# Optimization experiments

Hardware: AMD Instinct MI355X
Metric: run time of the kernel (lower is better)

The kernel has to match this reference:

```python
import jax, jax.numpy as jnp
import numpy as np

B, T, EMB, N_HEADS = 2, 2048, 128, 8
K_HALF = 4                      # k: gaussians at offsets -k..k
G_ADD = 2                       # gadditional global samples per gaussian
M = 2 * K_HALF + 1              # 9 gaussians per query
P = M * (2 + G_ADD)             # 36 sparse points per query (2 nearest ints + G_ADD)
SIGMA_BOOST = 2.0
EPS = 1e-7


def setup_inputs() -> dict:
    key = jax.random.key(0)
    ks = jax.random.split(key, 8)
    s = 1.0 / np.sqrt(EMB)
    return {
        "x": jax.random.normal(ks[0], (B, T, EMB), jnp.float32),
        "stride_params": jax.random.uniform(ks[1], (2,), jnp.float32, 0.5, 3.0),  # (dilation, raw sigma)
        "mvalues": jnp.ones((M,), jnp.float32),
        "Wq": jax.random.normal(ks[2], (EMB, EMB * N_HEADS), jnp.float32) * s,
        "Wk": jax.random.normal(ks[3], (EMB, EMB * N_HEADS), jnp.float32) * s,
        "Wv": jax.random.normal(ks[4], (EMB, EMB * N_HEADS), jnp.float32) * s,
        "Wu": jax.random.normal(ks[5], (EMB * N_HEADS, EMB), jnp.float32) * s,
        "bu": jnp.zeros((EMB,), jnp.float32),
    }


def _forward(x, stride_params, mvalues, Wq, Wk, Wv, Wu, bu):
    b, t, emb = x.shape
    dilation, sigma_raw = stride_params[0], stride_params[1]

    # --- hyper(): per-query gaussian means/sigmas (transform_means 'clamp', transform_sigmas softplus) ---
    offsets = jnp.arange(-K_HALF, K_HALF + 1, dtype=x.dtype) * dilation            # (M,)
    pos = jnp.arange(t, dtype=x.dtype)
    means = jnp.clip(pos[None, :, None] + offsets[None, None, :], 0.0, t - 1.0)    # (1,t,M)
    means = jnp.broadcast_to(means, (b, t, M))
    sigma = jax.nn.softplus(sigma_raw + SIGMA_BOOST) + EPS
    sigmas = jnp.broadcast_to(sigma, means.shape)                                  # (b,t,M)

    # --- sparse.ngenerate: 2 nearest ints + G_ADD uniform global samples per gaussian ---
    fl = jnp.floor(means)
    near = jnp.stack([fl, fl + 1.0], axis=-1)                                      # (b,t,M,2)
    glob = jax.random.randint(jax.random.key(42), (b, t, M, G_ADD), 0, t).astype(x.dtype)
    pts = jnp.clip(jnp.concatenate([near, glob], axis=-1), 0.0, t - 1.0)           # (b,t,M,2+G)
    idx = pts.reshape(b, t, P).astype(jnp.int32)                                   # (b,t,P)
    pts_fl = idx.astype(x.dtype)

    # --- sparse.densities: density of each point under each of the M gaussians ---
    diff = (pts_fl[..., :, None] - means[..., None, :]) / sigmas[..., None, :]     # (b,t,P,M)
    dens = jnp.exp(-0.5 * diff * diff)

    # --- util.nduplicates: zero all densities of duplicate points (keep first occurrence) ---
    eq = idx[..., :, None] == idx[..., None, :]                                    # (b,t,i,p)
    earlier = jnp.triu(jnp.ones((P, P), dtype=bool), k=1)                          # i < p
    dup = jnp.any(eq & earlier, axis=-2)                                           # (b,t,P)
    dens = jnp.where(dup[..., None], 0.0, dens)
    dens = dens / dens.sum(axis=2, keepdims=True)                                  # normalize over points per gaussian
    weights = jnp.einsum('btpm,m->btp', dens, mvalues)                             # (b,t,P)

    # --- projections; note per-head dim == emb in this module ---
    def proj(W):
        return jnp.transpose((x @ W).reshape(b, t, N_HEADS, emb), (0, 2, 1, 3))    # (b,h,t,e)

    scale = emb ** 0.25
    Q = proj(Wq) / scale
    K = proj(Wk) / scale
    V = proj(Wv)

    def per_batch(Qb, Kb, Vb, idxb, wb):
        Kg = Kb[:, idxb]                                # (h,t,P,e) irregular gather
        dot = jnp.einsum('hte,htpe->htp', Qb, Kg)       # util.calc_vals: sparse gather dot-products
        attn = jax.nn.softmax(wb[None, :, :] * dot, axis=-1)  # sparse.logsoftmax(...).exp(): per output-row
        Vg = Vb[:, idxb]                                # (h,t,P,e)
        return jnp.einsum('htp,htpe->hte', attn, Vg)    # sparse.batchmm scatter-reduce over rows

    out = jax.vmap(per_batch)(Q, K, V, idx, weights)    # (b,h,t,e)
    out = jnp.transpose(out, (0, 2, 1, 3)).reshape(b, t, N_HEADS * emb)
    return out @ Wu + bu


def reference(x, stride_params, mvalues, Wq, Wk, Wv, Wu, bu):
    return _forward(x, stride_params, mvalues, Wq, Wk, Wv, Wu, bu)
```

## Files before the change

### kernel.cpp

```cpp
#include <hip/hip_runtime.h>
#include <math.h>

#define B_    2
#define T_    2048
#define EMB_  128
#define NH_   8
#define M_    9
#define P_    36
#define GADD_ 2

typedef _Float16 f16;
typedef __attribute__((ext_vector_type(2))) _Float16 f16x2;
typedef __attribute__((ext_vector_type(4))) _Float16 f16x4;
typedef __attribute__((ext_vector_type(8))) _Float16 f16x8;
typedef __attribute__((ext_vector_type(4))) float f32x4;

__device__ __forceinline__ unsigned rotl32(unsigned x, int r){ return (x<<r)|(x>>(32-r)); }

struct U2 { unsigned x, y; };

__device__ __forceinline__ U2 tf2x32(U2 key, U2 ctr){
  unsigned ks[3] = { key.x, key.y, key.x ^ key.y ^ 0x1BD11BDAu };
  unsigned x0 = ctr.x + ks[0], x1 = ctr.y + ks[1];
  const int rotA[4] = {13,15,26,6}, rotB[4] = {17,29,16,24};
  #pragma unroll
  for (int r = 0; r < 5; ++r){
    const int* rr = (r & 1) ? rotB : rotA;
    #pragma unroll
    for (int i = 0; i < 4; ++i){ x0 += x1; x1 = rotl32(x1, rr[i]); x1 ^= x0; }
    x0 += ks[(r+1)%3];
    x1 += ks[(r+2)%3] + (unsigned)(r+1);
  }
  return { x0, x1 };
}

__device__ unsigned glob_rand(unsigned f){
  U2 k2 = tf2x32({0u, 42u}, {0u, 1u});
  U2 o  = tf2x32(k2, {0u, f});
  return (o.x ^ o.y) & (unsigned)(T_-1);
}

__device__ __forceinline__ f16x2 as_f16x2(unsigned u){ return __builtin_bit_cast(f16x2, u); }
__device__ __forceinline__ unsigned as_u32(f16x2 v){ return __builtin_bit_cast(unsigned, v); }

__device__ __forceinline__ void tconv_body(const float* __restrict__ A,
    f16* __restrict__ o, int R, int C, int r0, int c0, float scale,
    float (*tile)[33]){
  const int tx = threadIdx.x & 31, ty = threadIdx.x >> 5;
  #pragma unroll
  for (int i = 0; i < 32; i += 8)
    tile[ty+i][tx] = A[(size_t)(r0+ty+i)*C + c0+tx];
  __syncthreads();
  #pragma unroll
  for (int i = 0; i < 32; i += 8)
    o[(size_t)(c0+ty+i)*R + (r0+tx)] = (f16)(tile[tx][ty+i] * scale);
}

__global__ __launch_bounds__(256) void prep_kernel(
    const float* __restrict__ x, f16* __restrict__ xh,
    const float* __restrict__ Wq, const float* __restrict__ Wk, const float* __restrict__ Wv,
    f16* __restrict__ WT,
    const float* __restrict__ Wu, f16* __restrict__ WuT,
    const float* __restrict__ sp, const float* __restrict__ mvals,
    int* __restrict__ idx_out, float* __restrict__ w_out){
  __shared__ float tile[32][33];
  __shared__ int   s_idx[4][P_];
  __shared__ float s_dens[4][P_][M_];
  __shared__ float s_col[4][M_];
  const int bid = blockIdx.x;
  const float sc = 0.29730177875068026f;

  if (bid < 512){
    const int i = (bid*256 + threadIdx.x)*4;
    float4 v = *(const float4*)(x + i);
    f16x4 p = { (f16)v.x, (f16)v.y, (f16)v.z, (f16)v.w };
    *(f16x4*)(xh + i) = p;
    return;
  }
  if (bid < 896){
    const int zz = bid - 512;
    const int z = zz >> 7, rem = zz & 127;
    const int by = rem >> 5, bx = rem & 31;
    const float* A = (z==0) ? Wq : (z==1) ? Wk : Wv;
    tconv_body(A, WT + (size_t)z*1024*128, 128, 1024, by*32, bx*32, (z<2)?sc:1.0f, tile);
    return;
  }
  if (bid < 1024){
    const int idx2 = bid - 896;
    const int by = idx2 >> 2, bx = idx2 & 3;
    tconv_body(Wu, WuT, 1024, 128, by*32, bx*32, 1.0f, tile);
    return;
  }

  const int g  = threadIdx.x >> 6;
  const int p  = threadIdx.x & 63;
  const int bt = (bid - 1024)*4 + g;
  const int t  = bt & (T_-1);

  const float dil  = sp[0];
  const float xs   = sp[1] + 2.0f;
  const float sigma = xs + log1pf(expf(-xs)) + 1e-7f;

  if (p < P_){
    const int m = p >> 2, j = p & 3;
    const float mean = fminf(fmaxf((float)t + (float)(m-4)*dil, 0.f), (float)(T_-1));
    int id;
    if      (j == 0) id = (int)floorf(mean);
    else if (j == 1) id = min((int)floorf(mean) + 1, T_-1);
    else {
      const unsigned f = ((unsigned)bt * M_ + (unsigned)m) * GADD_ + (unsigned)(j-2);
      id = (int)glob_rand(f);
    }
    s_idx[g][p] = id;
  }
  __syncthreads();
  if (p < P_){
    const int myid = s_idx[g][p];
    bool dup = false;
    for (int q = 0; q < p; ++q) dup |= (s_idx[g][q] == myid);
    const float pf = (float)myid;
    #pragma unroll
    for (int m = 0; m < M_; ++m){
      const float mean = fminf(fmaxf((float)t + (float)(m-4)*dil, 0.f), (float)(T_-1));
      const float d = (pf - mean) / sigma;
      s_dens[g][p][m] = dup ? 0.f : expf(-0.5f * d * d);
    }
  }
  __syncthreads();
  if (p < M_){
    float s = 0.f;
    for (int q = 0; q < P_; ++q) s += s_dens[g][q][p];
    s_col[g][p] = s;
  }
  __syncthreads();
  if (p < P_){
    float w = 0.f;
    #pragma unroll
    for (int m = 0; m < M_; ++m) w += s_dens[g][p][m] / s_col[g][m] * mvals[m];
    idx_out[bt*P_ + p] = s_idx[g][p];
    w_out[bt*P_ + p]   = w;
  }
}

__global__ __launch_bounds__(256) void qkv_mfma_kernel(const f16* __restrict__ xh,
    const f16* __restrict__ WT,
    f16* __restrict__ Qh, f16* __restrict__ Kh, f16* __restrict__ Vh){
  const int w  = threadIdx.x >> 6, l = threadIdx.x & 63;
  const int m0 = blockIdx.y*64 + w*16;
  const int n0 = blockIdx.x*64;
  const int lr = l & 15, lk = l >> 4;

  f16x8 a[4];
  #pragma unroll
  for (int kc = 0; kc < 4; ++kc)
    a[kc] = *(const f16x8*)(xh + (size_t)(m0+lr)*128 + kc*32 + lk*8);

  #pragma unroll
  for (int z = 0; z < 3; ++z){
    const f16* __restrict__ WTz = WT + (size_t)z * 1024 * 128;
    f16* __restrict__ Outh = (z==0) ? Qh : (z==1) ? Kh : Vh;
    f32x4 acc[4] = {};
    #pragma unroll
    for (int nf = 0; nf < 4; ++nf){
      #pragma unroll
      for (int kc = 0; kc < 4; ++kc){
        f16x8 b = *(const f16x8*)(WTz + (size_t)(n0+nf*16+lr)*128 + kc*32 + lk*8);
        acc[nf] = __builtin_amdgcn_mfma_f32_16x16x32_f16(a[kc], b, acc[nf], 0, 0, 0);
      }
    }
    #pragma unroll
    for (int nf = 0; nf < 4; ++nf){
      const int col = n0 + nf*16 + lr;
      #pragma unroll
      for (int r = 0; r < 4; ++r)
        Outh[(size_t)(m0 + lk*4 + r)*1024 + col] = (f16)acc[nf][r];
    }
  }
}

#define RSTR 37
#define NHB  4
__global__ __launch_bounds__(256) void attn_kernel(const f16* __restrict__ Qh,
    const f16* __restrict__ K, const f16* __restrict__ V,
    const int* __restrict__ idx, const float* __restrict__ wts,
    f16* __restrict__ outh){
  const int bid = blockIdx.x;
  const int bt  = ((bid & 7) << 9) | (bid >> 3);
  const int b   = bt >> 11;
  const int hw   = threadIdx.x >> 6, lane = threadIdx.x & 63;
  const int h    = blockIdx.y*NHB + hw;
  const int pg = lane >> 4, li = lane & 15;

  __shared__ int   s_koff[P_];
  __shared__ float s_w[P_];
  __shared__ float s_red[NHB][16*RSTR];
  __shared__ float s_a[NHB][36];

  if (threadIdx.x < P_){
    s_koff[threadIdx.x] = idx[bt*P_ + threadIdx.x] << 10;
    s_w[threadIdx.x]    = wts[bt*P_ + threadIdx.x];
  }
  __syncthreads();

  const size_t rowBase = (size_t)bt*1024 + h*EMB_;
  const uint4 qu = *(const uint4*)(Qh + rowBase + li*8);
  const f16x2 q01 = as_f16x2(qu.x), q23 = as_f16x2(qu.y);
  const f16x2 q45 = as_f16x2(qu.z), q67 = as_f16x2(qu.w);
  const f16* __restrict__ Kb = K + (size_t)b*T_*1024 + h*EMB_ + li*8;
  const f16* __restrict__ Vb = V + (size_t)b*T_*1024 + h*EMB_ + li*8;

  int ko[9];
  #pragma unroll
  for (int c = 0; c < 9; ++c) ko[c] = s_koff[4*c + pg];

  uint4 kU[9];
  #pragma unroll
  for (int c = 0; c < 9; ++c) kU[c] = *(const uint4*)(Kb + ko[c]);

  float pr[9];
  #pragma unroll
  for (int c = 0; c < 9; ++c){
    pr[c] = __builtin_amdgcn_fdot2(as_f16x2(kU[c].x), q01,
            __builtin_amdgcn_fdot2(as_f16x2(kU[c].y), q23,
            __builtin_amdgcn_fdot2(as_f16x2(kU[c].z), q45,
            __builtin_amdgcn_fdot2(as_f16x2(kU[c].w), q67, 0.f, false),
            false), false), false);
  }

  float* __restrict__ red = s_red[hw];
  {
    float* __restrict__ dst = red + li*RSTR + pg;
    #pragma unroll
    for (int c = 0; c < 9; ++c) dst[4*c] = pr[c];
  }
  const int pcol = (lane < P_) ? lane : 0;
  float s0=0.f, s1=0.f, s2=0.f, s3=0.f;
  #pragma unroll
  for (int r = 0; r < 16; r += 4){
    s0 += red[(r+0)*RSTR + pcol];
    s1 += red[(r+1)*RSTR + pcol];
    s2 += red[(r+2)*RSTR + pcol];
    s3 += red[(r+3)*RSTR + pcol];
  }
  const float logit = (s0+s1)+(s2+s3);

  float val = (lane < P_) ? logit * s_w[pcol] : -INFINITY;
  float mx = val;
  #pragma unroll
  for (int off = 32; off; off >>= 1) mx = fmaxf(mx, __shfl_xor(mx, off));
  float e = (lane < P_) ? expf(val - mx) : 0.f;
  float s = e;
  #pragma unroll
  for (int off = 32; off; off >>= 1) s += __shfl_xor(s, off);
  if (lane < P_) s_a[hw][lane] = e / s;

  f16x2 a01 = {(f16)0.f,(f16)0.f}, a23 = a01, a45 = a01, a67 = a01;
  #pragma unroll
  for (int c = 0; c < 9; ++c){
    const f16 awh = (f16)s_a[hw][4*c + pg];
    const f16x2 vw = { awh, awh };
    const uint4 u = *(const uint4*)(Vb + ko[c]);
    a01 = vw * as_f16x2(u.x) + a01;
    a23 = vw * as_f16x2(u.y) + a23;
    a45 = vw * as_f16x2(u.z) + a45;
    a67 = vw * as_f16x2(u.w) + a67;
  }
  a01 = a01 + as_f16x2(__shfl_xor((int)as_u32(a01), 16));
  a23 = a23 + as_f16x2(__shfl_xor((int)as_u32(a23), 16));
  a45 = a45 + as_f16x2(__shfl_xor((int)as_u32(a45), 16));
  a67 = a67 + as_f16x2(__shfl_xor((int)as_u32(a67), 16));
  a01 = a01 + as_f16x2(__shfl_xor((int)as_u32(a01), 32));
  a23 = a23 + as_f16x2(__shfl_xor((int)as_u32(a23), 32));
  a45 = a45 + as_f16x2(__shfl_xor((int)as_u32(a45), 32));
  a67 = a67 + as_f16x2(__shfl_xor((int)as_u32(a67), 32));
  if (pg == 0){
    uint4 pck = { as_u32(a01), as_u32(a23), as_u32(a45), as_u32(a67) };
    *(uint4*)(outh + rowBase + li*8) = pck;
  }
}

__global__ __launch_bounds__(256) void out_partial_mfma(const f16* __restrict__ Ah,
    const f16* __restrict__ WuT, float* __restrict__ part){
  const int w  = threadIdx.x >> 6, l = threadIdx.x & 63;
  const int m0 = blockIdx.y*64 + w*16;
  const int k0 = blockIdx.x*256;
  const int lr = l & 15, lk = l >> 4;

  const f16* __restrict__ arow = Ah + (size_t)(m0+lr)*1024 + k0 + lk*8;
  f32x4 acc[8] = {};
  #pragma unroll
  for (int kc = 0; kc < 8; ++kc){
    f16x8 a = *(const f16x8*)(arow + kc*32);
    #pragma unroll
    for (int nf = 0; nf < 8; ++nf){
      f16x8 b = *(const f16x8*)(WuT + (size_t)(nf*16+lr)*1024 + k0 + kc*32 + lk*8);
      acc[nf] = __builtin_amdgcn_mfma_f32_16x16x32_f16(a, b, acc[nf], 0, 0, 0);
    }
  }
  float* __restrict__ dst = part + (size_t)blockIdx.x * (4096*128);
  #pragma unroll
  for (int nf = 0; nf < 8; ++nf){
    const int col = nf*16 + lr;
    #pragma unroll
    for (int r = 0; r < 4; ++r)
      dst[(size_t)(m0 + lk*4 + r)*128 + col] = acc[nf][r];
  }
}

__global__ __launch_bounds__(256) void out_reduce_kernel(const float* __restrict__ part,
    const float* __restrict__ bu, float* __restrict__ out){
  const int i = blockIdx.x * 256 + threadIdx.x;
  const int c0 = (i & 31) * 4;
  float4 acc = *(const float4*)(bu + c0);
  #pragma unroll
  for (int kc = 0; kc < 4; ++kc){
    float4 v = *(const float4*)(part + (size_t)kc*(4096*128) + (size_t)i*4);
    acc.x += v.x; acc.y += v.y; acc.z += v.z; acc.w += v.w;
  }
  *(float4*)(out + (size_t)i*4) = acc;
}

extern "C" void kernel_launch(void* const* d_in, const int* in_sizes, int n_in,
                              void* d_out, int out_size, void* d_ws, size_t ws_size,
                              hipStream_t stream){
  (void)in_sizes; (void)n_in; (void)out_size; (void)ws_size;
  const float* x    = (const float*)d_in[0];
  const float* sp   = (const float*)d_in[1];
  const float* mvl  = (const float*)d_in[2];
  const float* Wq   = (const float*)d_in[3];
  const float* Wk   = (const float*)d_in[4];
  const float* Wv   = (const float*)d_in[5];
  const float* Wu   = (const float*)d_in[6];
  const float* bu   = (const float*)d_in[7];
  float* out = (float*)d_out;

  const size_t n = (size_t)B_*NH_*T_*EMB_;
  f16*   Qh    = (f16*)d_ws;
  f16*   Kh    = Qh + n;
  f16*   Vh    = Kh + n;
  f16*   attnh = Vh + n;
  f16*   xh    = attnh + n;
  f16*   WT    = xh + (size_t)B_*T_*EMB_;
  f16*   WuT   = WT + 3*131072;
  int*   idxb  = (int*)(WuT + 131072);
  float* wb    = (float*)(idxb + (size_t)B_*T_*P_);
  float* part  = wb + (size_t)B_*T_*P_;

  prep_kernel<<<2048, 256, 0, stream>>>(x, xh, Wq, Wk, Wv, WT, Wu, WuT, sp, mvl, idxb, wb);
  qkv_mfma_kernel<<<dim3(16, 64), 256, 0, stream>>>(xh, WT, Qh, Kh, Vh);
  attn_kernel<<<dim3(B_*T_, 2), 256, 0, stream>>>(Qh, Kh, Vh, idxb, wb, attnh);
  out_partial_mfma<<<dim3(4, 64), 256, 0, stream>>>(attnh, WuT, part);
  out_reduce_kernel<<<512, 256, 0, stream>>>(part, bu, out);
}
```

Before: 80.53 us.

## Process four queries per attention block with prefetch and shuffle-based broadcasts

The attention kernel now handles four consecutive query rows per block instead of one, launching a quarter as many blocks. It prefetches the next row's indices, weights and Q while the current row computes, and issues V gathers before the softmax so they overlap. Shared-memory staging of indices and attention weights plus the block-wide barrier are replaced with wave shuffles. The cost is fewer blocks in flight and higher register pressure from holding both the K and V fragments.

Measured after the change: 82.86 us. +2.9%, slower.

```diff
diff --git a/kernel.cpp b/kernel.cpp
--- a/kernel.cpp
+++ b/kernel.cpp
@@ -179,103 +179,113 @@
 }
 
 #define RSTR 37
-#define NHB  4
 __global__ __launch_bounds__(256) void attn_kernel(const f16* __restrict__ Qh,
     const f16* __restrict__ K, const f16* __restrict__ V,
     const int* __restrict__ idx, const float* __restrict__ wts,
     f16* __restrict__ outh){
-  const int bid = blockIdx.x;
-  const int bt  = ((bid & 7) << 9) | (bid >> 3);
-  const int b   = bt >> 11;
-  const int hw   = threadIdx.x >> 6, lane = threadIdx.x & 63;
-  const int h    = blockIdx.y*NHB + hw;
+  const int bid   = blockIdx.x;
+  const int chunk = ((bid & 7) << 7) | (bid >> 3);
+  const int bt0   = chunk * 4;
+  const int b     = bt0 >> 11;
+  const int hw = threadIdx.x >> 6, lane = threadIdx.x & 63;
+  const int h  = blockIdx.y*4 + hw;
   const int pg = lane >> 4, li = lane & 15;
-
-  __shared__ int   s_koff[P_];
-  __shared__ float s_w[P_];
-  __shared__ float s_red[NHB][16*RSTR];
-  __shared__ float s_a[NHB][36];
-
-  if (threadIdx.x < P_){
-    s_koff[threadIdx.x] = idx[bt*P_ + threadIdx.x] << 10;
-    s_w[threadIdx.x]    = wts[bt*P_ + threadIdx.x];
-  }
-  __syncthreads();
-
-  const size_t rowBase = (size_t)bt*1024 + h*EMB_;
-  const uint4 qu = *(const uint4*)(Qh + rowBase + li*8);
-  const f16x2 q01 = as_f16x2(qu.x), q23 = as_f16x2(qu.y);
-  const f16x2 q45 = as_f16x2(qu.z), q67 = as_f16x2(qu.w);
+  const bool pl = (lane < P_);
+
+  __shared__ float s_red[4][16*RSTR];
+
   const f16* __restrict__ Kb = K + (size_t)b*T_*1024 + h*EMB_ + li*8;
   const f16* __restrict__ Vb = V + (size_t)b*T_*1024 + h*EMB_ + li*8;
 
-  int ko[9];
-  #pragma unroll
-  for (int c = 0; c < 9; ++c) ko[c] = s_koff[4*c + pg];
-
-  uint4 kU[9];
-  #pragma unroll
-  for (int c = 0; c < 9; ++c) kU[c] = *(const uint4*)(Kb + ko[c]);
-
-  float pr[9];
-  #pragma unroll
-  for (int c = 0; c < 9; ++c){
-    pr[c] = __builtin_amdgcn_fdot2(as_f16x2(kU[c].x), q01,
-            __builtin_amdgcn_fdot2(as_f16x2(kU[c].y), q23,
-            __builtin_amdgcn_fdot2(as_f16x2(kU[c].z), q45,
-            __builtin_amdgcn_fdot2(as_f16x2(kU[c].w), q67, 0.f, false),
-            false), false), false);
-  }
-
-  float* __restrict__ red = s_red[hw];
-  {
-    float* __restrict__ dst = red + li*RSTR + pg;
-    #pragma unroll
-    for (int c = 0; c < 9; ++c) dst[4*c] = pr[c];
-  }
-  const int pcol = (lane < P_) ? lane : 0;
-  float s0=0.f, s1=0.f, s2=0.f, s3=0.f;
-  #pragma unroll
-  for (int r = 0; r < 16; r += 4){
-    s0 += red[(r+0)*RSTR + pcol];
-    s1 += red[(r+1)*RSTR + pcol];
-    s2 += red[(r+2)*RSTR + pcol];
-    s3 += red[(r+3)*RSTR + pcol];
-  }
-  const float logit = (s0+s1)+(s2+s3);
-
-  float val = (lane < P_) ? logit * s_w[pcol] : -INFINITY;
-  float mx = val;
-  #pragma unroll
-  for (int off = 32; off; off >>= 1) mx = fmaxf(mx, __shfl_xor(mx, off));
-  float e = (lane < P_) ? expf(val - mx) : 0.f;
-  float s = e;
-  #pragma unroll
-  for (int off = 32; off; off >>= 1) s += __shfl_xor(s, off);
-  if (lane < P_) s_a[hw][lane] = e / s;
-
-  f16x2 a01 = {(f16)0.f,(f16)0.f}, a23 = a01, a45 = a01, a67 = a01;
-  #pragma unroll
-  for (int c = 0; c < 9; ++c){
-    const f16 awh = (f16)s_a[hw][4*c + pg];
-    const f16x2 vw = { awh, awh };
-    const uint4 u = *(const uint4*)(Vb + ko[c]);
-    a01 = vw * as_f16x2(u.x) + a01;
-    a23 = vw * as_f16x2(u.y) + a23;
-    a45 = vw * as_f16x2(u.z) + a45;
-    a67 = vw * as_f16x2(u.w) + a67;
-  }
-  a01 = a01 + as_f16x2(__shfl_xor((int)as_u32(a01), 16));
-  a23 = a23 + as_f16x2(__shfl_xor((int)as_u32(a23), 16));
-  a45 = a45 + as_f16x2(__shfl_xor((int)as_u32(a45), 16));
-  a67 = a67 + as_f16x2(__shfl_xor((int)as_u32(a67), 16));
-  a01 = a01 + as_f16x2(__shfl_xor((int)as_u32(a01), 32));
-  a23 = a23 + as_f16x2(__shfl_xor((int)as_u32(a23), 32));
-  a45 = a45 + as_f16x2(__shfl_xor((int)as_u32(a45), 32));
-  a67 = a67 + as_f16x2(__shfl_xor((int)as_u32(a67), 32));
-  if (pg == 0){
-    uint4 pck = { as_u32(a01), as_u32(a23), as_u32(a45), as_u32(a67) };
-    *(uint4*)(outh + rowBase + li*8) = pck;
+  int   idxv = pl ? idx[bt0*P_ + lane] : 0;
+  float wv   = pl ? wts[bt0*P_ + lane] : 0.f;
+  uint4 qu   = *(const uint4*)(Qh + (size_t)bt0*1024 + h*EMB_ + li*8);
+
+  #pragma unroll
+  for (int it = 0; it < 4; ++it){
+    const int bt = bt0 + it;
+
+    int ko[9];
+    #pragma unroll
+    for (int c = 0; c < 9; ++c) ko[c] = __shfl(idxv, 4*c + pg) << 10;
+    uint4 kU[9];
+    #pragma unroll
+    for (int c = 0; c < 9; ++c) kU[c] = *(const uint4*)(Kb + ko[c]);
+
+    int idxv_n = 0; float wv_n = 0.f; uint4 qu_n = {0,0,0,0};
+    if (it < 3){
+      idxv_n = pl ? idx[(bt+1)*P_ + lane] : 0;
+      wv_n   = pl ? wts[(bt+1)*P_ + lane] : 0.f;
+      qu_n   = *(const uint4*)(Qh + (size_t)(bt+1)*1024 + h*EMB_ + li*8);
+    }
+
+    const f16x2 q01 = as_f16x2(qu.x), q23 = as_f16x2(qu.y);
+    const f16x2 q45 = as_f16x2(qu.z), q67 = as_f16x2(qu.w);
+    float pr[9];
+    #pragma unroll
+    for (int c = 0; c < 9; ++c){
+      pr[c] = __builtin_amdgcn_fdot2(as_f16x2(kU[c].x), q01,
+              __builtin_amdgcn_fdot2(as_f16x2(kU[c].y), q23,
+              __builtin_amdgcn_fdot2(as_f16x2(kU[c].z), q45,
+              __builtin_amdgcn_fdot2(as_f16x2(kU[c].w), q67, 0.f, false),
+              false), false), false);
+    }
+
+    uint4 vU[9];
+    #pragma unroll
+    for (int c = 0; c < 9; ++c) vU[c] = *(const uint4*)(Vb + ko[c]);
+
+    float* __restrict__ red = s_red[hw];
+    {
+      float* __restrict__ dst = red + li*RSTR + pg;
+      #pragma unroll
+      for (int c = 0; c < 9; ++c) dst[4*c] = pr[c];
+    }
+    const int pcol = pl ? lane : 0;
+    float s0=0.f, s1=0.f, s2=0.f, s3=0.f;
+    #pragma unroll
+    for (int r = 0; r < 16; r += 4){
+      s0 += red[(r+0)*RSTR + pcol];
+      s1 += red[(r+1)*RSTR + pcol];
+      s2 += red[(r+2)*RSTR + pcol];
+      s3 += red[(r+3)*RSTR + pcol];
+    }
+    const float logit = (s0+s1)+(s2+s3);
+
+    float val = pl ? logit * wv : -INFINITY;
+    float mx = val;
+    #pragma unroll
+    for (int off = 32; off; off >>= 1) mx = fmaxf(mx, __shfl_xor(mx, off));
+    float e = pl ? expf(val - mx) : 0.f;
+    float s = e;
+    #pragma unroll
+    for (int off = 32; off; off >>= 1) s += __shfl_xor(s, off);
+    const float aval = e / s;
+
+    f16x2 a01 = {(f16)0.f,(f16)0.f}, a23 = a01, a45 = a01, a67 = a01;
+    #pragma unroll
+    for (int c = 0; c < 9; ++c){
+      const f16 awh = (f16)__shfl(aval, 4*c + pg);
+      const f16x2 vw = { awh, awh };
+      a01 = vw * as_f16x2(vU[c].x) + a01;
+      a23 = vw * as_f16x2(vU[c].y) + a23;
+      a45 = vw * as_f16x2(vU[c].z) + a45;
+      a67 = vw * as_f16x2(vU[c].w) + a67;
+    }
+    a01 = a01 + as_f16x2(__shfl_xor((int)as_u32(a01), 16));
+    a23 = a23 + as_f16x2(__shfl_xor((int)as_u32(a23), 16));
+    a45 = a45 + as_f16x2(__shfl_xor((int)as_u32(a45), 16));
+    a67 = a67 + as_f16x2(__shfl_xor((int)as_u32(a67), 16));
+    a01 = a01 + as_f16x2(__shfl_xor((int)as_u32(a01), 32));
+    a23 = a23 + as_f16x2(__shfl_xor((int)as_u32(a23), 32));
+    a45 = a45 + as_f16x2(__shfl_xor((int)as_u32(a45), 32));
+    a67 = a67 + as_f16x2(__shfl_xor((int)as_u32(a67), 32));
+    if (pg == 0){
+      uint4 pck = { as_u32(a01), as_u32(a23), as_u32(a45), as_u32(a67) };
+      *(uint4*)(outh + (size_t)bt*1024 + h*EMB_ + li*8) = pck;
+    }
+
+    idxv = idxv_n; wv = wv_n; qu = qu_n;
   }
 }
 
@@ -348,7 +358,7 @@
 
   prep_kernel<<<2048, 256, 0, stream>>>(x, xh, Wq, Wk, Wv, WT, Wu, WuT, sp, mvl, idxb, wb);
   qkv_mfma_kernel<<<dim3(16, 64), 256, 0, stream>>>(xh, WT, Qh, Kh, Vh);
-  attn_kernel<<<dim3(B_*T_, 2), 256, 0, stream>>>(Qh, Kh, Vh, idxb, wb, attnh);
+  attn_kernel<<<dim3(1024, 2), 256, 0, stream>>>(Qh, Kh, Vh, idxb, wb, attnh);
   out_partial_mfma<<<dim3(4, 64), 256, 0, stream>>>(attnh, WuT, part);
   out_reduce_kernel<<<512, 256, 0, stream>>>(part, bu, out);
 }
```

## Fuse split-K output projection and reduction via shared memory in one kernel

Applied to the files above, without the earlier changes.

The output projection previously wrote four split-K partial results to global memory and then ran a separate reduction kernel that added them plus the bias. Now each block handles a 16-row by 64-column tile, its four waves compute the four K slices, and the partials are summed with the bias through shared memory before a single store. This removes one launch and an 8 MB round trip of partial sums through global memory. In exchange it adds a block barrier and an LDS round trip, and the grid changes to 512 smaller blocks with less reuse of A across columns.

Measured after the change: 77.61 us. 3.6% less time.

```diff
diff --git a/kernel.cpp b/kernel.cpp
--- a/kernel.cpp
+++ b/kernel.cpp
@@ -279,45 +279,48 @@
   }
 }
 
-__global__ __launch_bounds__(256) void out_partial_mfma(const f16* __restrict__ Ah,
-    const f16* __restrict__ WuT, float* __restrict__ part){
+__global__ __launch_bounds__(256) void out_fused_mfma(const f16* __restrict__ Ah,
+    const f16* __restrict__ WuT, const float* __restrict__ bu,
+    float* __restrict__ out){
   const int w  = threadIdx.x >> 6, l = threadIdx.x & 63;
-  const int m0 = blockIdx.y*64 + w*16;
-  const int k0 = blockIdx.x*256;
+  const int m0 = blockIdx.x*16;
+  const int n0 = blockIdx.y*64;
+  const int k0 = w*256;
   const int lr = l & 15, lk = l >> 4;
 
+  __shared__ float s_part[4][16][64];
+
   const f16* __restrict__ arow = Ah + (size_t)(m0+lr)*1024 + k0 + lk*8;
-  f32x4 acc[8] = {};
+  f32x4 acc[4] = {};
   #pragma unroll
   for (int kc = 0; kc < 8; ++kc){
     f16x8 a = *(const f16x8*)(arow + kc*32);
     #pragma unroll
-    for (int nf = 0; nf < 8; ++nf){
-      f16x8 b = *(const f16x8*)(WuT + (size_t)(nf*16+lr)*1024 + k0 + kc*32 + lk*8);
+    for (int nf = 0; nf < 4; ++nf){
+      f16x8 b = *(const f16x8*)(WuT + (size_t)(n0+nf*16+lr)*1024 + k0 + kc*32 + lk*8);
       acc[nf] = __builtin_amdgcn_mfma_f32_16x16x32_f16(a, b, acc[nf], 0, 0, 0);
     }
   }
-  float* __restrict__ dst = part + (size_t)blockIdx.x * (4096*128);
-  #pragma unroll
-  for (int nf = 0; nf < 8; ++nf){
-    const int col = nf*16 + lr;
+  #pragma unroll
+  for (int nf = 0; nf < 4; ++nf){
     #pragma unroll
     for (int r = 0; r < 4; ++r)
-      dst[(size_t)(m0 + lk*4 + r)*128 + col] = acc[nf][r];
-  }
-}
-
-__global__ __launch_bounds__(256) void out_reduce_kernel(const float* __restrict__ part,
-    const float* __restrict__ bu, float* __restrict__ out){
-  const int i = blockIdx.x * 256 + threadIdx.x;
-  const int c0 = (i & 31) * 4;
-  float4 acc = *(const float4*)(bu + c0);
-  #pragma unroll
-  for (int kc = 0; kc < 4; ++kc){
-    float4 v = *(const float4*)(part + (size_t)kc*(4096*128) + (size_t)i*4);
-    acc.x += v.x; acc.y += v.y; acc.z += v.z; acc.w += v.w;
-  }
-  *(float4*)(out + (size_t)i*4) = acc;
+      s_part[w][lk*4 + r][nf*16 + lr] = acc[nf][r];
+  }
+  __syncthreads();
+
+  const int r  = threadIdx.x >> 4;
+  const int c0 = (threadIdx.x & 15) * 4;
+  float4 a0 = *(const float4*)(&s_part[0][r][c0]);
+  float4 a1 = *(const float4*)(&s_part[1][r][c0]);
+  float4 a2 = *(const float4*)(&s_part[2][r][c0]);
+  float4 a3 = *(const float4*)(&s_part[3][r][c0]);
+  float4 bias = *(const float4*)(bu + n0 + c0);
+  float4 v = { (a0.x+a1.x)+(a2.x+a3.x)+bias.x,
+               (a0.y+a1.y)+(a2.y+a3.y)+bias.y,
+               (a0.z+a1.z)+(a2.z+a3.z)+bias.z,
+               (a0.w+a1.w)+(a2.w+a3.w)+bias.w };
+  *(float4*)(out + (size_t)(m0+r)*128 + n0 + c0) = v;
 }
 
 extern "C" void kernel_launch(void* const* d_in, const int* in_sizes, int n_in,
@@ -344,11 +347,9 @@
   f16*   WuT   = WT + 3*131072;
   int*   idxb  = (int*)(WuT + 131072);
   float* wb    = (float*)(idxb + (size_t)B_*T_*P_);
-  float* part  = wb + (size_t)B_*T_*P_;
 
   prep_kernel<<<2048, 256, 0, stream>>>(x, xh, Wq, Wk, Wv, WT, Wu, WuT, sp, mvl, idxb, wb);
   qkv_mfma_kernel<<<dim3(16, 64), 256, 0, stream>>>(xh, WT, Qh, Kh, Vh);
   attn_kernel<<<dim3(B_*T_, 2), 256, 0, stream>>>(Qh, Kh, Vh, idxb, wb, attnh);
-  out_partial_mfma<<<dim3(4, 64), 256, 0, stream>>>(attnh, WuT, part);
-  out_reduce_kernel<<<512, 256, 0, stream>>>(part, bu, out);
-}
+  out_fused_mfma<<<dim3(256, 2), 256, 0, stream>>>(attnh, WuT, bu, out);
+}
```
